# Performance work log

Measured on AMD Instinct MI355X. Metric: run time of the kernel, lower is better.

The kernel has to match this reference:

```python
import jax, jax.numpy as jnp
from jax import lax
import numpy as np

T, K, KEND = 2048, 4, 8
D, H, WD = 100, 256, 300
V, DICT, C = 20000, 700000, 18


def _build_end_indexed(starts, lens, ids, valid):
    # Group gazetteer words by their END position (the step at which the
    # lattice char cell consumes the word memory cell), padded to KEND slots.
    e_ids = np.zeros((T, KEND), np.int32)
    e_start = np.zeros((T, KEND), np.int32)
    e_mask = np.zeros((T, KEND), np.int32)
    cnt = np.zeros(T, np.int64)
    for t in range(T):
        for k in range(K):
            if valid[t, k]:
                e = int(starts[t, k] + lens[t, k] - 1)
                if cnt[e] < KEND:
                    e_ids[e, cnt[e]] = ids[t, k]
                    e_start[e, cnt[e]] = starts[t, k]
                    e_mask[e, cnt[e]] = 1
                    cnt[e] += 1
    return jnp.asarray(e_ids), jnp.asarray(e_start), jnp.asarray(e_mask)


def setup_inputs():
    ks = jax.random.split(jax.random.key(0), 24)
    inputs = jax.random.randint(ks[0], (1, T), 0, V, dtype=jnp.int32)
    rng = np.random.default_rng(0)
    lens = rng.integers(0, 8, size=(T, K))          # word length; valid iff >= 2
    ids = rng.integers(1, DICT, size=(T, K))        # gazetteer word ids
    pos = np.broadcast_to(np.arange(T)[:, None], (T, K))
    # forward direction: word starts at t, ends at t+len-1
    valid_f = (lens >= 2) & (pos + lens - 1 < T)
    fw_ids, fw_start, fw_mask = _build_end_indexed(pos, lens, ids, valid_f)
    # backward direction, expressed in the flipped frame: start' = T-1-(t+len-1)
    starts_b = T - 1 - (pos + lens - 1)
    valid_b = (lens >= 2) & (starts_b >= 0)
    bw_ids, bw_start, bw_mask = _build_end_indexed(starts_b, lens, ids, valid_b)
    s = 0.08
    nrm = lambda k, shape: jax.random.normal(k, shape, jnp.float32) * s
    p = {}
    i = 1
    for pre in ("fw", "bw"):
        p[pre + "_W_ih"] = nrm(ks[i], (D, 3 * H)); i += 1
        p[pre + "_W_hh"] = nrm(ks[i], (H, 3 * H)); i += 1
        p[pre + "_b"] = jnp.zeros((3 * H,), jnp.float32)
        p[pre + "_aW_ih"] = nrm(ks[i], (D, H)); i += 1
        p[pre + "_aW_hh"] = nrm(ks[i], (H, H)); i += 1
        p[pre + "_ab"] = jnp.zeros((H,), jnp.float32)
        p[pre + "_wW_ih"] = nrm(ks[i], (WD, 3 * H)); i += 1
        p[pre + "_wW_hh"] = nrm(ks[i], (H, 3 * H)); i += 1
        p[pre + "_wb"] = jnp.zeros((3 * H,), jnp.float32)
    out = dict(inputs=inputs, fw_ids=fw_ids, fw_start=fw_start, fw_mask=fw_mask,
               bw_ids=bw_ids, bw_start=bw_start, bw_mask=bw_mask, length=T,
               E=nrm(ks[20], (V, D)), word_table=nrm(ks[21], (DICT, WD)),
               W_lin=nrm(ks[22], (2 * H, C)), b_lin=jnp.zeros((C,), jnp.float32))
    out.update(p)
    return out


def _lattice_pass(x, wemb, start, mask, W_ih, W_hh, b, aW_ih, aW_hh, ab, wW_ih, wW_hh, wb):
    # x: [T,D]; wemb: [T,KEND,WD]; start/mask: [T,KEND]
    Tn, Hn = x.shape[0], W_hh.shape[0]

    def step(carry, xs):
        h, c, Hh, Ch = carry                        # Hh/Ch: [T,H] history of char states
        t, xt, we_t, st, m = xs
        mf = m.astype(x.dtype)[:, None]             # [KEND,1]
        hs, cs = Hh[st], Ch[st]                     # char state at each word's start pos
        # WordLSTMCell: c^w = sigmoid(f)*c_start + sigmoid(i)*tanh(g)
        wi, wf, wg = jnp.split(we_t @ wW_ih + hs @ wW_hh + wb, 3, axis=-1)
        cw = jax.nn.sigmoid(wf) * cs + jax.nn.sigmoid(wi) * jnp.tanh(wg)
        # MultiInputLSTMCell char gates
        ii, oo, gg = jnp.split(xt @ W_ih + h @ W_hh + b, 3, axis=-1)
        i_s, o_s, g_t = jax.nn.sigmoid(ii), jax.nn.sigmoid(oo), jnp.tanh(gg)
        # extra input gate per word, then exp-normalization over {i, alphas}
        alpha = jax.nn.sigmoid(xt @ aW_ih + cw @ aW_hh + ab)   # [KEND,H]
        e_i = jnp.exp(i_s)                                      # [H]
        e_a = jnp.exp(alpha) * mf                               # masked slots drop out
        c_merge = (e_i * g_t + (e_a * cw).sum(0)) / (e_i + e_a.sum(0))
        c_plain = (1.0 - i_s) * c + i_s * g_t                   # no-word branch (f = 1-i)
        c_new = jnp.where(jnp.any(m > 0), c_merge, c_plain)
        h_new = o_s * jnp.tanh(c_new)
        return (h_new, c_new, Hh.at[t].set(h_new), Ch.at[t].set(c_new)), h_new

    z = lambda *sh: jnp.zeros(sh, x.dtype)
    init = (z(Hn), z(Hn), z(Tn, Hn), z(Tn, Hn))
    _, hseq = lax.scan(step, init, (jnp.arange(Tn), x, wemb, start, mask))
    return hseq                                      # [T,H]


def reference(inputs, fw_ids, fw_start, fw_mask, bw_ids, bw_start, bw_mask, length, E,
              word_table, W_lin, b_lin,
              fw_W_ih, fw_W_hh, fw_b, fw_aW_ih, fw_aW_hh, fw_ab, fw_wW_ih, fw_wW_hh, fw_wb,
              bw_W_ih, bw_W_hh, bw_b, bw_aW_ih, bw_aW_hh, bw_ab, bw_wW_ih, bw_wW_hh, bw_wb):
    x = E[inputs[0]]                                 # [T,D] char embeddings (batch=1)
    hf = _lattice_pass(x, word_table[fw_ids], fw_start, fw_mask,
                       fw_W_ih, fw_W_hh, fw_b, fw_aW_ih, fw_aW_hh, fw_ab,
                       fw_wW_ih, fw_wW_hh, fw_wb)
    hb = _lattice_pass(x[::-1], word_table[bw_ids], bw_start, bw_mask,
                       bw_W_ih, bw_W_hh, bw_b, bw_aW_ih, bw_aW_hh, bw_ab,
                       bw_wW_ih, bw_wW_hh, bw_wb)[::-1]
    return (jnp.concatenate([hf, hb], axis=-1) @ W_lin + b_lin)[None]  # [1,T,C]
```

## Files before the change

### kernel.cpp

```cpp
#include <hip/hip_runtime.h>
#include <hip/hip_bf16.h>


#define TSEQ 2048
#define KEND 8
#define DEMB 100
#define H    256
#define H3   768
#define WD   300
#define CCLS 18
#define NTH  256

typedef __attribute__((ext_vector_type(8))) short bf16x8;
typedef __attribute__((ext_vector_type(4))) float f32x4;

#define LO_AT  0
#define LO_A1  131072
#define LO_UR  131584
#define LO_RC  142336
#define LO_PRE 150528
#define LO_A2  153600
#define LO_AWS 157824
#define LO_MT  161920
#define SMEM_SCAN 162176

__device__ __forceinline__ float sigf(float x) { return 1.0f / (1.0f + expf(-x)); }
__device__ __forceinline__ float bf2f(unsigned u) { return __uint_as_float(u << 16); }
__device__ __forceinline__ unsigned f2bf(float f) {
  union { float f; unsigned u; } x; x.f = f;
  unsigned r = x.u + 0x7fffu + ((x.u >> 16) & 1u);
  return r >> 16;
}

__global__ __launch_bounds__(64) void k_pack(
    const float* __restrict__ W_hh_f, const float* __restrict__ wW_hh_f, const float* __restrict__ aW_hh_f,
    const float* __restrict__ W_hh_b, const float* __restrict__ wW_hh_b, const float* __restrict__ aW_hh_b,
    unsigned short* __restrict__ Wpk)
{
  const int T = blockIdx.x, dir = blockIdx.y;
  const int lane = threadIdx.x;
  const float* Wg = dir ? W_hh_b  : W_hh_f;
  const float* Ww = dir ? wW_hh_b : wW_hh_f;
  const float* Wa = dir ? aW_hh_b : aW_hh_f;
  for (int ks = 0; ks < 8; ++ks) {
    bf16x8 sv;
#pragma unroll
    for (int e = 0; e < 8; ++e) {
      const int k = ks * 32 + (lane >> 4) * 8 + e;
      float f;
      if (T < 96) {
        const int c = T * 16 + (lane & 15);
        f = (c < H3) ? Wg[(size_t)k * H3 + c] : Ww[(size_t)k * H3 + (c - H3)];
      } else {
        const int c = (T - 96) * 16 + (lane & 15);
        f = Wa[(size_t)k * H + c];
      }
      sv[e] = (short)f2bf(f);
    }
    *(bf16x8*)(Wpk + (((size_t)dir * 112 + T) * 8 + ks) * 512 + lane * 8) = sv;
  }
}

__global__ __launch_bounds__(256) void k_embed(
    const int* __restrict__ inputs, const float* __restrict__ E,
    const float* __restrict__ W_ih_f, const float* __restrict__ b_f,
    const float* __restrict__ aW_ih_f, const float* __restrict__ ab_f,
    const float* __restrict__ W_ih_b, const float* __restrict__ b_b,
    const float* __restrict__ aW_ih_b, const float* __restrict__ ab_b,
    __hip_bfloat16* __restrict__ xg, float* __restrict__ xa)
{
  const int t = blockIdx.x, dir = blockIdx.y;
  const int tid = threadIdx.x;
  const float* W_ih = dir ? W_ih_b : W_ih_f;
  const float* bb   = dir ? b_b    : b_f;
  const float* aW   = dir ? aW_ih_b : aW_ih_f;
  const float* ab   = dir ? ab_b   : ab_f;
  const int src = dir ? (TSEQ - 1 - t) : t;

  __shared__ float xr[DEMB];
  if (tid < DEMB) xr[tid] = E[(size_t)inputs[src] * DEMB + tid];
  __syncthreads();

  float a0 = bb[tid], a1 = bb[H + tid], a2 = bb[2 * H + tid], a3 = ab[tid];
  for (int r = 0; r < DEMB; r += 4) {
    const float4 e4 = *reinterpret_cast<const float4*>(&xr[r]);
    const float ev[4] = {e4.x, e4.y, e4.z, e4.w};
#pragma unroll
    for (int kk = 0; kk < 4; ++kk) {
      const float* wp = W_ih + (size_t)(r + kk) * H3 + tid;
      a0 += ev[kk] * wp[0];
      a1 += ev[kk] * wp[H];
      a2 += ev[kk] * wp[2 * H];
      a3 += ev[kk] * aW[(size_t)(r + kk) * H + tid];
    }
  }
  __hip_bfloat16* xgrow = xg + ((size_t)dir * TSEQ + t) * H3;
  xgrow[tid]         = __float2bfloat16(a0);
  xgrow[H + tid]     = __float2bfloat16(a1);
  xgrow[2 * H + tid] = __float2bfloat16(a2);
  xa[((size_t)dir * TSEQ + t) * H + tid] = a3;
}

__global__ __launch_bounds__(256) void k_wordgates(
    const int* __restrict__ fw_ids, const int* __restrict__ fw_mask,
    const int* __restrict__ bw_ids, const int* __restrict__ bw_mask,
    const float* __restrict__ word_table,
    const float* __restrict__ wW_ih_f, const float* __restrict__ wb_f,
    const float* __restrict__ wW_ih_b, const float* __restrict__ wb_b,
    __hip_bfloat16* __restrict__ wg)
{
  const int t = blockIdx.x, dir = blockIdx.y;
  const int tid = threadIdx.x;
  const int* ids = (dir ? bw_ids : fw_ids) + t * KEND;
  const int* msk = (dir ? bw_mask : fw_mask) + t * KEND;
  const float* wW = dir ? wW_ih_b : wW_ih_f;
  const float* wb = dir ? wb_b    : wb_f;

  __shared__ float we[KEND][WD];
  for (int w = 0; w < KEND; ++w) {
    if (msk[w]) {
      const float* src = word_table + (size_t)ids[w] * WD;
      for (int i = tid; i < WD; i += 256) we[w][i] = src[i];
    }
  }
  __syncthreads();

  __hip_bfloat16* out = wg + ((size_t)dir * TSEQ + t) * KEND * H3;
  for (int w = 0; w < KEND; ++w) {
    if (!msk[w]) continue;
    float a0 = wb[tid], a1 = wb[H + tid], a2 = wb[2 * H + tid];
    for (int r = 0; r < WD; r += 4) {
      const float4 e4 = *reinterpret_cast<const float4*>(&we[w][r]);
      const float ev[4] = {e4.x, e4.y, e4.z, e4.w};
#pragma unroll
      for (int kk = 0; kk < 4; ++kk) {
        const float* wp = wW + (size_t)(r + kk) * H3 + tid;
        a0 += ev[kk] * wp[0];
        a1 += ev[kk] * wp[H];
        a2 += ev[kk] * wp[2 * H];
      }
    }
    out[w * H3 + tid]         = __float2bfloat16(a0);
    out[w * H3 + H + tid]     = __float2bfloat16(a1);
    out[w * H3 + 2 * H + tid] = __float2bfloat16(a2);
  }
}

__global__ __launch_bounds__(NTH, 1) void k_scan(
    const __hip_bfloat16* __restrict__ xg, const float* __restrict__ xa,
    const __hip_bfloat16* __restrict__ wgG, float* __restrict__ hseq,
    const int* __restrict__ fw_start, const int* __restrict__ fw_mask,
    const int* __restrict__ bw_start, const int* __restrict__ bw_mask,
    const unsigned short* __restrict__ Wpk,
    unsigned long long* __restrict__ hx, unsigned long long* __restrict__ ux)
{
  const int gid = blockIdx.x;
  if (gid != 0 && gid != 1 && gid != 8 && gid != 9) return;
  const int dir  = gid & 1;
  const int side = gid >> 3;

  extern __shared__ char smem[];
  unsigned short* A1_16 = (unsigned short*)(smem + LO_A1);
  unsigned short* ur16  = (unsigned short*)(smem + LO_UR);
  float* ringC = (float*)(smem + LO_RC);
  float* preS  = (float*)(smem + LO_PRE);
  unsigned short* awS16 = (unsigned short*)(smem + LO_AWS);
  int* metaI = (int*)(smem + LO_MT);

  const int tid  = threadIdx.x;
  const int lane = tid & 63;
  const int wv   = tid >> 6;
  const int lmod = lane & 15;
  const int lgrp = lane >> 4;

  const char* WpkD = (const char*)(Wpk + (size_t)dir * 112 * 8 * 512);

  unsigned long long* hbuf = hx + (size_t)dir * 2 * 128;
  unsigned long long* ubuf = ux + (size_t)dir * 2 * 384;

  bf16x8 rW[12][8];
  {
    const char* rp = WpkD + (size_t)(side * 48 + wv * 12) * 8192 + lane * 16;
#pragma unroll
    for (int n = 0; n < 12; ++n)
#pragma unroll
      for (int ks = 0; ks < 8; ++ks)
        rW[n][ks] = *(const bf16x8*)(rp + (n * 8 + ks) * 1024);
  }

  if (side == 1) {
    __syncthreads();
    for (int t = 1; t < TSEQ; ++t) {
      if (tid < 128) {
        const unsigned long long* src = hbuf + (size_t)((t - 1) & 1) * 128;
        unsigned long long q;
        do { q = __hip_atomic_load(src + tid, __ATOMIC_RELAXED, __HIP_MEMORY_SCOPE_AGENT); }
        while ((unsigned)(q >> 32) != (unsigned)t);
        *(unsigned*)((char*)A1_16 + tid * 4) = (unsigned)q;
      }
      __syncthreads();
#pragma unroll
      for (int g = 0; g < 2; ++g) {
        f32x4 acc[6];
#pragma unroll
        for (int n = 0; n < 6; ++n) acc[n] = f32x4{0.f, 0.f, 0.f, 0.f};
#pragma unroll
        for (int ks = 0; ks < 8; ++ks) {
          const bf16x8 av = *(const bf16x8*)(smem + LO_A1 + ks * 64 + lgrp * 16);
#pragma unroll
          for (int n = 0; n < 6; ++n)
            acc[n] = __builtin_amdgcn_mfma_f32_16x16x32_bf16(av, rW[g * 6 + n][ks], acc[n], 0, 0, 0);
        }
#pragma unroll
        for (int n = 0; n < 6; ++n) {
          const unsigned hb = f2bf(acc[n][0]) & 0xffffu;
          const unsigned ob = (unsigned)__shfl_down((int)hb, 1) & 0xffffu;
          if (lane < 16 && !(lane & 1)) {
            const int tix = wv * 12 + g * 6 + n;
            const unsigned long long q =
                ((unsigned long long)(unsigned)t << 32) | (hb | (ob << 16));
            __hip_atomic_store(ubuf + (size_t)((t - 1) & 1) * 384 + tix * 8 + (lane >> 1), q,
                               __ATOMIC_RELAXED, __HIP_MEMORY_SCOPE_AGENT);
          }
        }
      }
      __syncthreads();
    }
    return;
  }

  const int* startA = dir ? bw_start : fw_start;
  const int* maskA  = dir ? bw_mask  : fw_mask;

  for (int o = tid * 16; o < 131072; o += NTH * 16)
    *(uint4*)(smem + LO_AT + o) = *(const uint4*)(WpkD + (size_t)96 * 8192 + o);
  if (tid < 32) *(uint4*)(smem + LO_A1 + tid * 16) = uint4{0, 0, 0, 0};
  for (int o = tid * 16; o < 4224; o += NTH * 16)
    *(uint4*)(smem + LO_A2 + o) = uint4{0, 0, 0, 0};
  for (int o = tid * 16; o < 8192; o += NTH * 16)
    *(uint4*)(smem + LO_RC + o) = uint4{0, 0, 0, 0};

  unsigned nxI = 0, nxO = 0, nxG = 0; float nxA = 0.f;
  unsigned cxI = 0, cxO = 0, cxG = 0; float cxA = 0.f;
  int nmt = 0;
  {
    const unsigned short* xr = (const unsigned short*)(xg + (size_t)dir * TSEQ * H3);
    nxI = xr[tid]; nxO = xr[H + tid]; nxG = xr[2 * H + tid];
    nxA = xa[(size_t)dir * TSEQ * H + tid];
    if (wv == 3) {
      if (lane < 8) nmt = maskA[lane];
      else if (lane < 16) nmt = startA[lane - 8];
    }
  }
  __syncthreads();
  if (wv == 3) {
    int mAll[8], sAll[8];
#pragma unroll
    for (int s = 0; s < 8; ++s) { mAll[s] = __shfl(nmt, s); sAll[s] = __shfl(nmt, 8 + s); }
    if (lane == 0) {
      int n = 0;
      for (int s = 0; s < 8; ++s)
        if (mAll[s]) { metaI[1 + n] = s; metaI[9 + n] = sAll[s]; ++n; }
      metaI[0] = n;
    }
  }
  cxI = nxI; cxO = nxO; cxG = nxG; cxA = nxA;
  __syncthreads();

  int uHave = -1;

  for (int t = 0; t < TSEQ; ++t) {
    const int par = t & 1;
    const int* mp = metaI + par * 32;
    const int nw = mp[0];
    int hasL2w = 0;
    for (int w = 0; w < nw; ++w) hasL2w |= (mp[9 + w] == t - 1);

    unsigned short wgv[24];
#pragma unroll
    for (int it = 0; it < 8; ++it) {
      const int u0 = tid + it * NTH;
      if (u0 < nw * 256) {
        const int w = u0 >> 8, j = u0 & 255;
        const int slot = mp[1 + w];
        const unsigned short* wgp =
            (const unsigned short*)wgG + ((size_t)(dir * TSEQ + t) * KEND + slot) * H3 + j;
        wgv[it * 3 + 0] = wgp[0];
        wgv[it * 3 + 1] = wgp[256];
        wgv[it * 3 + 2] = wgp[512];
      }
    }

#pragma unroll
    for (int g = 0; g < 2; ++g) {
      f32x4 acc[6];
#pragma unroll
      for (int n = 0; n < 6; ++n) acc[n] = f32x4{0.f, 0.f, 0.f, 0.f};
#pragma unroll
      for (int ks = 0; ks < 8; ++ks) {
        const bf16x8 av = *(const bf16x8*)(smem + LO_A1 + ks * 64 + lgrp * 16);
#pragma unroll
        for (int n = 0; n < 6; ++n)
          acc[n] = __builtin_amdgcn_mfma_f32_16x16x32_bf16(av, rW[g * 6 + n][ks], acc[n], 0, 0, 0);
      }
      if (lane < 16) {
#pragma unroll
        for (int n = 0; n < 6; ++n)
          preS[(wv * 12 + g * 6 + n) * 16 + lane] = acc[n][0];
      }
    }

    if (t >= 2 && uHave < t - 2) {
      const int s = t - 2;
      const unsigned long long* src = ubuf + (size_t)(s & 1) * 384;
      unsigned long long q;
      do { q = __hip_atomic_load(src + tid, __ATOMIC_RELAXED, __HIP_MEMORY_SCOPE_AGENT); }
      while ((unsigned)(q >> 32) != (unsigned)(s + 1));
      *(unsigned*)((char*)ur16 + (s % 7) * 1536 + tid * 4) = (unsigned)q;
      if (tid < 128) {
        do { q = __hip_atomic_load(src + 256 + tid, __ATOMIC_RELAXED, __HIP_MEMORY_SCOPE_AGENT); }
        while ((unsigned)(q >> 32) != (unsigned)(s + 1));
        *(unsigned*)((char*)ur16 + (s % 7) * 1536 + (256 + tid) * 4) = (unsigned)q;
      }
      uHave = t - 2;
    }

    {
      const int tn = (t + 1 < TSEQ) ? t + 1 : TSEQ - 1;
      const unsigned short* xr = (const unsigned short*)(xg + ((size_t)dir * TSEQ + tn) * H3);
      nxI = xr[tid]; nxO = xr[H + tid]; nxG = xr[2 * H + tid];
      nxA = xa[((size_t)dir * TSEQ + tn) * H + tid];
      if (wv == 3) {
        if (lane < 8) nmt = maskA[tn * KEND + lane];
        else if (lane < 16) nmt = startA[tn * KEND + (lane - 8)];
      }
    }
    __syncthreads();

#pragma unroll
    for (int it = 0; it < 8; ++it) {
      const int u0 = tid + it * NTH;
      if (u0 < nw * 256) {
        const int w = u0 >> 8, j = u0 & 255;
        const int s = mp[9 + w];
        if (s != t - 1) {
          const unsigned short* ur = ur16 + (s % 7) * 768;
          const float wi  = bf2f(wgv[it * 3 + 0]) + bf2f(ur[j]);
          const float wf  = bf2f(wgv[it * 3 + 1]) + bf2f(ur[256 + j]);
          const float wgg = bf2f(wgv[it * 3 + 2]) + bf2f(ur[512 + j]);
          const float cs  = ringC[(s & 7) * 256 + j];
          const float cv  = sigf(wf) * cs + sigf(wi) * tanhf(wgg);
          *(unsigned short*)(smem + LO_A2 + w * 528 + j * 2) = (unsigned short)f2bf(cv);
        }
      }
    }
    if (hasL2w) {
      {
        const int s = t - 1;
        const unsigned long long* src = ubuf + (size_t)(s & 1) * 384;
        unsigned long long q;
        do { q = __hip_atomic_load(src + tid, __ATOMIC_RELAXED, __HIP_MEMORY_SCOPE_AGENT); }
        while ((unsigned)(q >> 32) != (unsigned)(s + 1));
        *(unsigned*)((char*)ur16 + (s % 7) * 1536 + tid * 4) = (unsigned)q;
        if (tid < 128) {
          do { q = __hip_atomic_load(src + 256 + tid, __ATOMIC_RELAXED, __HIP_MEMORY_SCOPE_AGENT); }
          while ((unsigned)(q >> 32) != (unsigned)(s + 1));
          *(unsigned*)((char*)ur16 + (s % 7) * 1536 + (256 + tid) * 4) = (unsigned)q;
        }
        uHave = t - 1;
      }
      __syncthreads();
#pragma unroll
      for (int it = 0; it < 8; ++it) {
        const int u0 = tid + it * NTH;
        if (u0 < nw * 256) {
          const int w = u0 >> 8, j = u0 & 255;
          const int s = mp[9 + w];
          if (s == t - 1) {
            const unsigned short* ur = ur16 + (s % 7) * 768;
            const float wi  = bf2f(wgv[it * 3 + 0]) + bf2f(ur[j]);
            const float wf  = bf2f(wgv[it * 3 + 1]) + bf2f(ur[256 + j]);
            const float wgg = bf2f(wgv[it * 3 + 2]) + bf2f(ur[512 + j]);
            const float cs  = ringC[(s & 7) * 256 + j];
            const float cv  = sigf(wf) * cs + sigf(wi) * tanhf(wgg);
            *(unsigned short*)(smem + LO_A2 + w * 528 + j * 2) = (unsigned short)f2bf(cv);
          }
        }
      }
    }
    __syncthreads();

    if (nw > 0) {
      const int r2 = (lmod > 7) ? 7 : lmod;
      f32x4 ac[4];
#pragma unroll
      for (int m = 0; m < 4; ++m) ac[m] = f32x4{0.f, 0.f, 0.f, 0.f};
#pragma unroll
      for (int ks = 0; ks < 8; ++ks) {
        const bf16x8 a2v = *(const bf16x8*)(smem + LO_A2 + r2 * 528 + ks * 64 + lgrp * 16);
#pragma unroll
        for (int m = 0; m < 4; ++m) {
          const bf16x8 b = *(const bf16x8*)(smem + LO_AT + (size_t)(wv * 4 + m) * 8192 + ks * 1024 + lane * 16);
          ac[m] = __builtin_amdgcn_mfma_f32_16x16x32_bf16(a2v, b, ac[m], 0, 0, 0);
        }
      }
#pragma unroll
      for (int m = 0; m < 4; ++m) {
#pragma unroll
        for (int r = 0; r < 4; ++r) {
          const int row = lgrp * 4 + r;
          if (row < nw) awS16[row * 256 + (wv * 4 + m) * 16 + lmod] = (unsigned short)f2bf(ac[m][r]);
        }
      }
    }
    __syncthreads();

    {
      const int j = tid;
      const float i_s = sigf(bf2f(cxI) + preS[j]);
      const float o_s = sigf(bf2f(cxO) + preS[256 + j]);
      const float g_t = tanhf(bf2f(cxG) + preS[512 + j]);
      float cnew;
      if (nw > 0) {
        const float e_i = expf(i_s);
        float num = e_i * g_t, den = e_i;
        for (int w = 0; w < nw; ++w) {
          const float a  = sigf(cxA + bf2f(awS16[w * 256 + j]));
          const float ea = expf(a);
          num += ea * bf2f(*(const unsigned short*)(smem + LO_A2 + w * 528 + j * 2));
          den += ea;
        }
        cnew = num / den;
      } else {
        cnew = (1.f - i_s) * ringC[((t - 1) & 7) * 256 + j] + i_s * g_t;
      }
      const float hnew = o_s * tanhf(cnew);
      ringC[(t & 7) * 256 + j] = cnew;
      const unsigned hb = f2bf(hnew) & 0xffffu;
      A1_16[j] = (unsigned short)hb;
      hseq[((size_t)dir * TSEQ + t) * H + j] = hnew;
      const unsigned ob = (unsigned)__shfl_xor((int)hb, 1) & 0xffffu;
      if (!(tid & 1)) {
        const unsigned long long q =
            ((unsigned long long)(unsigned)(t + 1) << 32) | (hb | (ob << 16));
        __hip_atomic_store(hbuf + (size_t)par * 128 + (tid >> 1), q,
                           __ATOMIC_RELAXED, __HIP_MEMORY_SCOPE_AGENT);
      }
    }
    if (wv == 3) {
      int mAll[8], sAll[8];
#pragma unroll
      for (int s = 0; s < 8; ++s) { mAll[s] = __shfl(nmt, s); sAll[s] = __shfl(nmt, 8 + s); }
      if (lane == 0) {
        int* mq = metaI + ((t + 1) & 1) * 32;
        int n = 0;
        for (int s = 0; s < 8; ++s)
          if (mAll[s]) { mq[1 + n] = s; mq[9 + n] = sAll[s]; ++n; }
        mq[0] = n;
      }
    }
    cxI = nxI; cxO = nxO; cxG = nxG; cxA = nxA;
    __syncthreads();
  }
}

__global__ __launch_bounds__(64) void k_proj(
    const float* __restrict__ hseq, const float* __restrict__ W_lin,
    const float* __restrict__ b_lin, float* __restrict__ out)
{
  const int t = blockIdx.x;
  const int tid = threadIdx.x;
  __shared__ float hrow[2 * H];
  for (int i = tid; i < H; i += 64) {
    hrow[i]     = hseq[(size_t)t * H + i];
    hrow[H + i] = hseq[((size_t)TSEQ + (TSEQ - 1 - t)) * H + i];
  }
  __syncthreads();
  if (tid < CCLS) {
    float acc = b_lin[tid];
    for (int j = 0; j < 2 * H; ++j) acc += hrow[j] * W_lin[(size_t)j * CCLS + tid];
    out[(size_t)t * CCLS + tid] = acc;
  }
}

extern "C" void kernel_launch(void* const* d_in, const int* in_sizes, int n_in,
                              void* d_out, int out_size, void* d_ws, size_t ws_size,
                              hipStream_t stream)
{
  const int* inputs   = (const int*)d_in[0];
  const int* fw_ids   = (const int*)d_in[1];
  const int* fw_start = (const int*)d_in[2];
  const int* fw_mask  = (const int*)d_in[3];
  const int* bw_ids   = (const int*)d_in[4];
  const int* bw_start = (const int*)d_in[5];
  const int* bw_mask  = (const int*)d_in[6];
  const float* E          = (const float*)d_in[8];
  const float* word_table = (const float*)d_in[9];
  const float* W_lin      = (const float*)d_in[10];
  const float* b_lin      = (const float*)d_in[11];
  const float* fw_W_ih  = (const float*)d_in[12];
  const float* fw_W_hh  = (const float*)d_in[13];
  const float* fw_b     = (const float*)d_in[14];
  const float* fw_aW_ih = (const float*)d_in[15];
  const float* fw_aW_hh = (const float*)d_in[16];
  const float* fw_ab    = (const float*)d_in[17];
  const float* fw_wW_ih = (const float*)d_in[18];
  const float* fw_wW_hh = (const float*)d_in[19];
  const float* fw_wb    = (const float*)d_in[20];
  const float* bw_W_ih  = (const float*)d_in[21];
  const float* bw_W_hh  = (const float*)d_in[22];
  const float* bw_b     = (const float*)d_in[23];
  const float* bw_aW_ih = (const float*)d_in[24];
  const float* bw_aW_hh = (const float*)d_in[25];
  const float* bw_ab    = (const float*)d_in[26];
  const float* bw_wW_ih = (const float*)d_in[27];
  const float* bw_wW_hh = (const float*)d_in[28];
  const float* bw_wb    = (const float*)d_in[29];

  char* p = (char*)d_ws;
  __hip_bfloat16* xg = (__hip_bfloat16*)p;  p += (size_t)2 * TSEQ * H3 * 2;
  float* xa   = (float*)p;                  p += (size_t)2 * TSEQ * H * 4;
  float* hseq = (float*)p;                  p += (size_t)2 * TSEQ * H * 4;
  __hip_bfloat16* wg = (__hip_bfloat16*)p;  p += (size_t)2 * TSEQ * KEND * H3 * 2;
  unsigned short* Wpk = (unsigned short*)p; p += (size_t)2 * 112 * 8 * 512 * 2;
  unsigned long long* hx = (unsigned long long*)p; p += (size_t)2 * 2 * 128 * 8;
  unsigned long long* ux = (unsigned long long*)p; p += (size_t)2 * 2 * 384 * 8;

  hipFuncSetAttribute((const void*)k_scan,
                      hipFuncAttributeMaxDynamicSharedMemorySize, SMEM_SCAN);
  hipMemsetAsync(hx, 0, (size_t)2 * 2 * 128 * 8 + (size_t)2 * 2 * 384 * 8, stream);

  k_pack<<<dim3(112, 2), 64, 0, stream>>>(
      fw_W_hh, fw_wW_hh, fw_aW_hh, bw_W_hh, bw_wW_hh, bw_aW_hh, Wpk);
  k_embed<<<dim3(TSEQ, 2), 256, 0, stream>>>(
      inputs, E, fw_W_ih, fw_b, fw_aW_ih, fw_ab, bw_W_ih, bw_b, bw_aW_ih, bw_ab, xg, xa);
  k_wordgates<<<dim3(TSEQ, 2), 256, 0, stream>>>(
      fw_ids, fw_mask, bw_ids, bw_mask, word_table, fw_wW_ih, fw_wb, bw_wW_ih, bw_wb, wg);
  k_scan<<<16, NTH, SMEM_SCAN, stream>>>(
      xg, xa, wg, hseq, fw_start, fw_mask, bw_start, bw_mask, Wpk, hx, ux);
  k_proj<<<TSEQ, 64, 0, stream>>>(hseq, W_lin, b_lin, (float*)d_out);
}
```

Measured before the change: 16.33 ms.

## Replace per-element tagged polling with per-direction flag counters in scan handshake

The cross-block handshake between the two scan sides no longer embeds a step tag in every 64-bit payload word with each thread spinning on it. A single monotonic counter per direction and buffer is now published after a block barrier, and one thread polls it with s_sleep before the payload is read untagged. The word-cell update and gate-matrix section is also regrouped under a single nw>0 branch, which skips barriers on steps with no words. The risk is weaker ordering: both data and flag use relaxed stores with no release fence, so stale payloads could be observed. It also adds a second global round trip (flag, then data) on the critical path.

```diff
diff --git a/kernel.cpp b/kernel.cpp
--- a/kernel.cpp
+++ b/kernel.cpp
@@ -152,7 +152,8 @@
     const int* __restrict__ fw_start, const int* __restrict__ fw_mask,
     const int* __restrict__ bw_start, const int* __restrict__ bw_mask,
     const unsigned short* __restrict__ Wpk,
-    unsigned long long* __restrict__ hx, unsigned long long* __restrict__ ux)
+    unsigned long long* __restrict__ hx, unsigned long long* __restrict__ ux,
+    unsigned* __restrict__ xf)
 {
   const int gid = blockIdx.x;
   if (gid != 0 && gid != 1 && gid != 8 && gid != 9) return;
@@ -177,6 +178,8 @@
 
   unsigned long long* hbuf = hx + (size_t)dir * 2 * 128;
   unsigned long long* ubuf = ux + (size_t)dir * 2 * 384;
+  unsigned* hFlag = xf + dir * 64;
+  unsigned* uFlag = xf + dir * 64 + 32;
 
   bf16x8 rW[12][8];
   {
@@ -190,12 +193,15 @@
 
   if (side == 1) {
     __syncthreads();
-    for (int t = 1; t < TSEQ; ++t) {
+    for (int s = 0; s < TSEQ - 1; ++s) {
+      if (tid == 0) {
+        while (__hip_atomic_load(hFlag, __ATOMIC_RELAXED, __HIP_MEMORY_SCOPE_AGENT) < (unsigned)(s + 1))
+          __builtin_amdgcn_s_sleep(1);
+      }
+      __syncthreads();
       if (tid < 128) {
-        const unsigned long long* src = hbuf + (size_t)((t - 1) & 1) * 128;
-        unsigned long long q;
-        do { q = __hip_atomic_load(src + tid, __ATOMIC_RELAXED, __HIP_MEMORY_SCOPE_AGENT); }
-        while ((unsigned)(q >> 32) != (unsigned)t);
+        const unsigned long long q =
+            __hip_atomic_load(hbuf + (size_t)(s & 1) * 128 + tid, __ATOMIC_RELAXED, __HIP_MEMORY_SCOPE_AGENT);
         *(unsigned*)((char*)A1_16 + tid * 4) = (unsigned)q;
       }
       __syncthreads();
@@ -217,14 +223,15 @@
           const unsigned ob = (unsigned)__shfl_down((int)hb, 1) & 0xffffu;
           if (lane < 16 && !(lane & 1)) {
             const int tix = wv * 12 + g * 6 + n;
-            const unsigned long long q =
-                ((unsigned long long)(unsigned)t << 32) | (hb | (ob << 16));
-            __hip_atomic_store(ubuf + (size_t)((t - 1) & 1) * 384 + tix * 8 + (lane >> 1), q,
+            __hip_atomic_store(ubuf + (size_t)(s & 1) * 384 + tix * 8 + (lane >> 1),
+                               (unsigned long long)(hb | (ob << 16)),
                                __ATOMIC_RELAXED, __HIP_MEMORY_SCOPE_AGENT);
           }
         }
       }
       __syncthreads();
+      if (tid == 0)
+        __hip_atomic_store(uFlag, (unsigned)(s + 1), __ATOMIC_RELAXED, __HIP_MEMORY_SCOPE_AGENT);
     }
     return;
   }
@@ -310,21 +317,11 @@
       }
     }
 
-    if (t >= 2 && uHave < t - 2) {
-      const int s = t - 2;
-      const unsigned long long* src = ubuf + (size_t)(s & 1) * 384;
-      unsigned long long q;
-      do { q = __hip_atomic_load(src + tid, __ATOMIC_RELAXED, __HIP_MEMORY_SCOPE_AGENT); }
-      while ((unsigned)(q >> 32) != (unsigned)(s + 1));
-      *(unsigned*)((char*)ur16 + (s % 7) * 1536 + tid * 4) = (unsigned)q;
-      if (tid < 128) {
-        do { q = __hip_atomic_load(src + 256 + tid, __ATOMIC_RELAXED, __HIP_MEMORY_SCOPE_AGENT); }
-        while ((unsigned)(q >> 32) != (unsigned)(s + 1));
-        *(unsigned*)((char*)ur16 + (s % 7) * 1536 + (256 + tid) * 4) = (unsigned)q;
-      }
-      uHave = t - 2;
-    }
-
+    const int needA = (t >= 2 && uHave < t - 2);
+    if (needA && tid == 0) {
+      while (__hip_atomic_load(uFlag, __ATOMIC_RELAXED, __HIP_MEMORY_SCOPE_AGENT) < (unsigned)(t - 1))
+        __builtin_amdgcn_s_sleep(1);
+    }
     {
       const int tn = (t + 1 < TSEQ) ? t + 1 : TSEQ - 1;
       const unsigned short* xr = (const unsigned short*)(xg + ((size_t)dir * TSEQ + tn) * H3);
@@ -337,46 +334,32 @@
     }
     __syncthreads();
 
-#pragma unroll
-    for (int it = 0; it < 8; ++it) {
-      const int u0 = tid + it * NTH;
-      if (u0 < nw * 256) {
-        const int w = u0 >> 8, j = u0 & 255;
-        const int s = mp[9 + w];
-        if (s != t - 1) {
-          const unsigned short* ur = ur16 + (s % 7) * 768;
-          const float wi  = bf2f(wgv[it * 3 + 0]) + bf2f(ur[j]);
-          const float wf  = bf2f(wgv[it * 3 + 1]) + bf2f(ur[256 + j]);
-          const float wgg = bf2f(wgv[it * 3 + 2]) + bf2f(ur[512 + j]);
-          const float cs  = ringC[(s & 7) * 256 + j];
-          const float cv  = sigf(wf) * cs + sigf(wi) * tanhf(wgg);
-          *(unsigned short*)(smem + LO_A2 + w * 528 + j * 2) = (unsigned short)f2bf(cv);
-        }
-      }
-    }
-    if (hasL2w) {
+    if (needA) {
+      const int s = t - 2;
+      const unsigned long long* src = ubuf + (size_t)(s & 1) * 384;
       {
-        const int s = t - 1;
-        const unsigned long long* src = ubuf + (size_t)(s & 1) * 384;
-        unsigned long long q;
-        do { q = __hip_atomic_load(src + tid, __ATOMIC_RELAXED, __HIP_MEMORY_SCOPE_AGENT); }
-        while ((unsigned)(q >> 32) != (unsigned)(s + 1));
+        const unsigned long long q =
+            __hip_atomic_load(src + tid, __ATOMIC_RELAXED, __HIP_MEMORY_SCOPE_AGENT);
         *(unsigned*)((char*)ur16 + (s % 7) * 1536 + tid * 4) = (unsigned)q;
-        if (tid < 128) {
-          do { q = __hip_atomic_load(src + 256 + tid, __ATOMIC_RELAXED, __HIP_MEMORY_SCOPE_AGENT); }
-          while ((unsigned)(q >> 32) != (unsigned)(s + 1));
-          *(unsigned*)((char*)ur16 + (s % 7) * 1536 + (256 + tid) * 4) = (unsigned)q;
-        }
-        uHave = t - 1;
-      }
+      }
+      if (tid < 128) {
+        const unsigned long long q =
+            __hip_atomic_load(src + 256 + tid, __ATOMIC_RELAXED, __HIP_MEMORY_SCOPE_AGENT);
+        *(unsigned*)((char*)ur16 + (s % 7) * 1536 + (256 + tid) * 4) = (unsigned)q;
+      }
+      uHave = t - 2;
+    }
+
+    if (nw > 0) {
       __syncthreads();
+
 #pragma unroll
       for (int it = 0; it < 8; ++it) {
         const int u0 = tid + it * NTH;
         if (u0 < nw * 256) {
           const int w = u0 >> 8, j = u0 & 255;
           const int s = mp[9 + w];
-          if (s == t - 1) {
+          if (s != t - 1) {
             const unsigned short* ur = ur16 + (s % 7) * 768;
             const float wi  = bf2f(wgv[it * 3 + 0]) + bf2f(ur[j]);
             const float wf  = bf2f(wgv[it * 3 + 1]) + bf2f(ur[256 + j]);
@@ -387,33 +370,73 @@
           }
         }
       }
-    }
-    __syncthreads();
-
-    if (nw > 0) {
-      const int r2 = (lmod > 7) ? 7 : lmod;
-      f32x4 ac[4];
-#pragma unroll
-      for (int m = 0; m < 4; ++m) ac[m] = f32x4{0.f, 0.f, 0.f, 0.f};
-#pragma unroll
-      for (int ks = 0; ks < 8; ++ks) {
-        const bf16x8 a2v = *(const bf16x8*)(smem + LO_A2 + r2 * 528 + ks * 64 + lgrp * 16);
+      if (hasL2w) {
+        if (tid == 0) {
+          while (__hip_atomic_load(uFlag, __ATOMIC_RELAXED, __HIP_MEMORY_SCOPE_AGENT) < (unsigned)t)
+            __builtin_amdgcn_s_sleep(1);
+        }
+        __syncthreads();
+        {
+          const int s = t - 1;
+          const unsigned long long* src = ubuf + (size_t)(s & 1) * 384;
+          {
+            const unsigned long long q =
+                __hip_atomic_load(src + tid, __ATOMIC_RELAXED, __HIP_MEMORY_SCOPE_AGENT);
+            *(unsigned*)((char*)ur16 + (s % 7) * 1536 + tid * 4) = (unsigned)q;
+          }
+          if (tid < 128) {
+            const unsigned long long q =
+                __hip_atomic_load(src + 256 + tid, __ATOMIC_RELAXED, __HIP_MEMORY_SCOPE_AGENT);
+            *(unsigned*)((char*)ur16 + (s % 7) * 1536 + (256 + tid) * 4) = (unsigned)q;
+          }
+          uHave = t - 1;
+        }
+        __syncthreads();
+#pragma unroll
+        for (int it = 0; it < 8; ++it) {
+          const int u0 = tid + it * NTH;
+          if (u0 < nw * 256) {
+            const int w = u0 >> 8, j = u0 & 255;
+            const int s = mp[9 + w];
+            if (s == t - 1) {
+              const unsigned short* ur = ur16 + (s % 7) * 768;
+              const float wi  = bf2f(wgv[it * 3 + 0]) + bf2f(ur[j]);
+              const float wf  = bf2f(wgv[it * 3 + 1]) + bf2f(ur[256 + j]);
+              const float wgg = bf2f(wgv[it * 3 + 2]) + bf2f(ur[512 + j]);
+              const float cs  = ringC[(s & 7) * 256 + j];
+              const float cv  = sigf(wf) * cs + sigf(wi) * tanhf(wgg);
+              *(unsigned short*)(smem + LO_A2 + w * 528 + j * 2) = (unsigned short)f2bf(cv);
+            }
+          }
+        }
+      }
+      __syncthreads();
+
+      {
+        const int r2 = (lmod > 7) ? 7 : lmod;
+        f32x4 ac[4];
+#pragma unroll
+        for (int m = 0; m < 4; ++m) ac[m] = f32x4{0.f, 0.f, 0.f, 0.f};
+#pragma unroll
+        for (int ks = 0; ks < 8; ++ks) {
+          const bf16x8 a2v = *(const bf16x8*)(smem + LO_A2 + r2 * 528 + ks * 64 + lgrp * 16);
+#pragma unroll
+          for (int m = 0; m < 4; ++m) {
+            const bf16x8 b = *(const bf16x8*)(smem + LO_AT + (size_t)(wv * 4 + m) * 8192 + ks * 1024 + lane * 16);
+            ac[m] = __builtin_amdgcn_mfma_f32_16x16x32_bf16(a2v, b, ac[m], 0, 0, 0);
+          }
+        }
 #pragma unroll
         for (int m = 0; m < 4; ++m) {
-          const bf16x8 b = *(const bf16x8*)(smem + LO_AT + (size_t)(wv * 4 + m) * 8192 + ks * 1024 + lane * 16);
-          ac[m] = __builtin_amdgcn_mfma_f32_16x16x32_bf16(a2v, b, ac[m], 0, 0, 0);
-        }
-      }
-#pragma unroll
-      for (int m = 0; m < 4; ++m) {
-#pragma unroll
-        for (int r = 0; r < 4; ++r) {
-          const int row = lgrp * 4 + r;
-          if (row < nw) awS16[row * 256 + (wv * 4 + m) * 16 + lmod] = (unsigned short)f2bf(ac[m][r]);
-        }
-      }
-    }
-    __syncthreads();
+#pragma unroll
+          for (int r = 0; r < 4; ++r) {
+            const int row = lgrp * 4 + r;
+            if (row < nw) awS16[row * 256 + (wv * 4 + m) * 16 + lmod] = (unsigned short)f2bf(ac[m][r]);
+          }
+        }
+      }
+      __syncthreads();
+    }
 
     {
       const int j = tid;
@@ -440,12 +463,10 @@
       A1_16[j] = (unsigned short)hb;
       hseq[((size_t)dir * TSEQ + t) * H + j] = hnew;
       const unsigned ob = (unsigned)__shfl_xor((int)hb, 1) & 0xffffu;
-      if (!(tid & 1)) {
-        const unsigned long long q =
-            ((unsigned long long)(unsigned)(t + 1) << 32) | (hb | (ob << 16));
-        __hip_atomic_store(hbuf + (size_t)par * 128 + (tid >> 1), q,
+      if (!(tid & 1))
+        __hip_atomic_store(hbuf + (size_t)par * 128 + (tid >> 1),
+                           (unsigned long long)(hb | (ob << 16)),
                            __ATOMIC_RELAXED, __HIP_MEMORY_SCOPE_AGENT);
-      }
     }
     if (wv == 3) {
       int mAll[8], sAll[8];
@@ -461,6 +482,8 @@
     }
     cxI = nxI; cxO = nxO; cxG = nxG; cxA = nxA;
     __syncthreads();
+    if (tid == 0)
+      __hip_atomic_store(hFlag, (unsigned)(t + 1), __ATOMIC_RELAXED, __HIP_MEMORY_SCOPE_AGENT);
   }
 }
 
@@ -525,10 +548,11 @@
   unsigned short* Wpk = (unsigned short*)p; p += (size_t)2 * 112 * 8 * 512 * 2;
   unsigned long long* hx = (unsigned long long*)p; p += (size_t)2 * 2 * 128 * 8;
   unsigned long long* ux = (unsigned long long*)p; p += (size_t)2 * 2 * 384 * 8;
+  unsigned* xf = (unsigned*)p;              p += 512;
 
   hipFuncSetAttribute((const void*)k_scan,
                       hipFuncAttributeMaxDynamicSharedMemorySize, SMEM_SCAN);
-  hipMemsetAsync(hx, 0, (size_t)2 * 2 * 128 * 8 + (size_t)2 * 2 * 384 * 8, stream);
+  hipMemsetAsync(xf, 0, 512, stream);
 
   k_pack<<<dim3(112, 2), 64, 0, stream>>>(
       fw_W_hh, fw_wW_hh, fw_aW_hh, bw_W_hh, bw_wW_hh, bw_aW_hh, Wpk);
@@ -537,6 +561,6 @@
   k_wordgates<<<dim3(TSEQ, 2), 256, 0, stream>>>(
       fw_ids, fw_mask, bw_ids, bw_mask, word_table, fw_wW_ih, fw_wb, bw_wW_ih, bw_wb, wg);
   k_scan<<<16, NTH, SMEM_SCAN, stream>>>(
-      xg, xa, wg, hseq, fw_start, fw_mask, bw_start, bw_mask, Wpk, hx, ux);
+      xg, xa, wg, hseq, fw_start, fw_mask, bw_start, bw_mask, Wpk, hx, ux, xf);
   k_proj<<<TSEQ, 64, 0, stream>>>(hseq, W_lin, b_lin, (float*)d_out);
 }
```

After: 16.66 ms. 1.02x slower.
